# Optimization experiments

Measured on AMD Instinct MI355X. Metric: run time of the kernel, lower is better.

The kernel has to match this reference:

```python
import jax, jax.numpy as jnp
import numpy as np

DILATION = 1
THETA = 1.0
K = 3 + 2 * (DILATION - 1)  # 3x3 window


def setup_inputs() -> dict:
    key = jax.random.key(0)
    x = jax.random.normal(key, (8, 64, 224, 224), dtype=jnp.float32)
    return {"x": x}


def _extract_patches(x, k, d):
    # x: [b, c, h, w] -> patches: [b, c, k*k, h, w], zero-padded like F.unfold(padding=d)
    b, c, h, w = x.shape
    xp = jnp.pad(x, ((0, 0), (0, 0), (d, d), (d, d)))
    return jnp.stack(
        [xp[:, :, i * d:i * d + h, j * d:j * d + w] for i in range(k) for j in range(k)],
        axis=2,
    )


def reference(x) -> jnp.ndarray:
    b, c, h, w = x.shape
    patches = _extract_patches(x, K, DILATION)  # [b, c, kk, h, w]

    mean = patches.mean(axis=2, keepdims=True)
    # torch .std() is unbiased (ddof=1)
    std = jnp.clip(jnp.std(patches, axis=2, keepdims=True, ddof=1), 1e-3, None)
    normed = (patches - mean) / std

    contrast = (normed ** 2).mean(axis=2)
    energy = (patches ** 2).mean(axis=2)
    clamped = jnp.clip(patches, 1e-6, None)
    entropy = -(clamped * jnp.log(clamped)).mean(axis=2)
    homogeneity = 1.0 / ((1.0 + jnp.abs(patches - mean)).mean(axis=2) + 1e-6)

    feats = jnp.stack([contrast, energy, entropy, homogeneity], axis=2)  # [b, c, 4, h, w]

    log_feat = jnp.log(jnp.clip(feats, 1e-5, None))
    martingale = jnp.clip(jnp.exp(THETA * log_feat - 0.5 * THETA ** 2), 1e-4, 1e4)
    martingale = jnp.where(jnp.isfinite(martingale), martingale, jnp.ones_like(martingale))

    # per-channel feature stacks concatenated along channel dim -> [b, c*4, h, w]
    return martingale.reshape(b, c * 4, h, w)
```

## Files before the change

kernel.cpp:

```cpp
#include <hip/hip_runtime.h>
#include <math.h>

#define B 8
#define C 64
#define H 224
#define W 224
#define TW 32
#define TH 8

__global__ __launch_bounds__(256) void medseg_kernel(const float* __restrict__ x,
                                                     float* __restrict__ out) {
    __shared__ float tile[(TH + 2)][(TW + 2)];

    const int plane = blockIdx.z;
    const int w0 = blockIdx.x * TW;
    const int h0 = blockIdx.y * TH;
    const float* __restrict__ xp = x + (size_t)plane * (H * W);

    const int tid = threadIdx.x;

    #pragma unroll
    for (int i = tid; i < (TH + 2) * (TW + 2); i += 256) {
        const int r  = i / (TW + 2);
        const int cc = i - r * (TW + 2);
        const int hh = h0 + r - 1;
        const int ww = w0 + cc - 1;
        float v = 0.0f;
        if (hh >= 0 && hh < H && ww >= 0 && ww < W) v = xp[hh * W + ww];
        tile[r][cc] = v;
    }
    __syncthreads();

    const int tx = tid & (TW - 1);
    const int ty = tid >> 5;

    float v[9];
    #pragma unroll
    for (int i = 0; i < 3; ++i)
        #pragma unroll
        for (int j = 0; j < 3; ++j)
            v[i * 3 + j] = tile[ty + i][tx + j];

    float s1 = 0.0f, s2 = 0.0f;
    #pragma unroll
    for (int k = 0; k < 9; ++k) {
        s1 += v[k];
        s2 = fmaf(v[k], v[k], s2);
    }
    const float mean = s1 * (1.0f / 9.0f);

    float s2c = 0.0f, sad = 0.0f;
    #pragma unroll
    for (int k = 0; k < 9; ++k) {
        const float d = v[k] - mean;
        s2c = fmaf(d, d, s2c);
        sad += fabsf(d);
    }

    float st = 0.0f;
    #pragma unroll
    for (int k = 0; k < 9; ++k) {
        const float c = fmaxf(v[k], 1e-6f);
        st = fmaf(c, __logf(c), st);
    }

    const float var  = s2c * (1.0f / 8.0f);
    const float stdc = fmaxf(__fsqrt_rn(var), 1e-3f);

    const float contrast = (s2c / (stdc * stdc)) * (1.0f / 9.0f);
    const float energy   = s2 * (1.0f / 9.0f);
    const float entropy  = -st * (1.0f / 9.0f);
    const float homog    = 1.0f / (1.0f + sad * (1.0f / 9.0f) + 1e-6f);

    const float EXPM = 0.6065306597126334f;
    float m[4];
    m[0] = contrast; m[1] = energy; m[2] = entropy; m[3] = homog;
    #pragma unroll
    for (int f = 0; f < 4; ++f) {
        float mm = fmaxf(m[f], 1e-5f) * EXPM;
        mm = fminf(fmaxf(mm, 1e-4f), 1e4f);
        if (!isfinite(mm)) mm = 1.0f;
        m[f] = mm;
    }

    const size_t base = ((size_t)plane * 4) * (size_t)(H * W)
                      + (size_t)(h0 + ty) * W + (w0 + tx);
    #pragma unroll
    for (int f = 0; f < 4; ++f) {
        out[base + (size_t)f * (H * W)] = m[f];
    }
}

extern "C" void kernel_launch(void* const* d_in, const int* in_sizes, int n_in,
                              void* d_out, int out_size, void* d_ws, size_t ws_size,
                              hipStream_t stream) {
    const float* x = (const float*)d_in[0];
    float* out = (float*)d_out;
    dim3 grid(W / TW, H / TH, B * C);
    dim3 block(TW * TH);
    medseg_kernel<<<grid, block, 0, stream>>>(x, out);
}
```

Before: 554.2 us.

## Compute four outputs per thread with register sliding window and float4 I/O

Drops the shared-memory tile and barrier. Each thread now loads three float4 chunks per row for three rows straight into registers and computes four horizontally adjacent outputs. Column sums of values, squares and x·log(x) are shared between neighbouring windows, so the per-element log is computed once per column rather than once per window. Outputs are written as float4. The cost is more redundant global loads for halos and higher register pressure, with launch_bounds set to 4 blocks.

```diff
diff --git a/kernel.cpp b/kernel.cpp
--- a/kernel.cpp
+++ b/kernel.cpp
@@ -5,90 +5,93 @@
 #define C 64
 #define H 224
 #define W 224
+#define HW (H * W)
 #define TW 32
-#define TH 8
+#define TH 32
 
-__global__ __launch_bounds__(256) void medseg_kernel(const float* __restrict__ x,
-                                                     float* __restrict__ out) {
-    __shared__ float tile[(TH + 2)][(TW + 2)];
-
+__global__ __launch_bounds__(256, 4) void medseg_kernel(const float* __restrict__ x,
+                                                        float* __restrict__ out) {
     const int plane = blockIdx.z;
     const int w0 = blockIdx.x * TW;
     const int h0 = blockIdx.y * TH;
-    const float* __restrict__ xp = x + (size_t)plane * (H * W);
+    const int tid = threadIdx.x;
+    const int tx = tid & 7;
+    const int ty = tid >> 3;
 
-    const int tid = threadIdx.x;
+    const float* __restrict__ xp = x + (size_t)plane * HW;
+
+    const int cb = w0 + 4 * tx;
+    const int h  = h0 + ty;
+
+    float win[3][12];
+    const float4 Z = make_float4(0.f, 0.f, 0.f, 0.f);
+    #pragma unroll
+    for (int i = 0; i < 3; ++i) {
+        const int r = h - 1 + i;
+        const bool rin = (r >= 0) && (r < H);
+        const float* rowp = xp + r * W;
+        float4 a = (rin && cb > 0)     ? *(const float4*)(rowp + cb - 4) : Z;
+        float4 b = rin                 ? *(const float4*)(rowp + cb)     : Z;
+        float4 c = (rin && cb + 4 < W) ? *(const float4*)(rowp + cb + 4) : Z;
+        win[i][0] = a.x; win[i][1]  = a.y; win[i][2]  = a.z; win[i][3]  = a.w;
+        win[i][4] = b.x; win[i][5]  = b.y; win[i][6]  = b.z; win[i][7]  = b.w;
+        win[i][8] = c.x; win[i][9]  = c.y; win[i][10] = c.z; win[i][11] = c.w;
+    }
+
+    float cs[6], cq[6], ce[6];
+    #pragma unroll
+    for (int j = 0; j < 6; ++j) {
+        const float v0 = win[0][j + 3], v1 = win[1][j + 3], v2 = win[2][j + 3];
+        cs[j] = v0 + v1 + v2;
+        cq[j] = fmaf(v0, v0, fmaf(v1, v1, v2 * v2));
+        const float c0 = fmaxf(v0, 1e-6f), c1 = fmaxf(v1, 1e-6f), c2 = fmaxf(v2, 1e-6f);
+        ce[j] = fmaf(c0, __logf(c0), fmaf(c1, __logf(c1), c2 * __logf(c2)));
+    }
+
+    const float EXPM = 0.6065306597126334f;
+    float oc[4], oe[4], ot[4], oh[4];
 
     #pragma unroll
-    for (int i = tid; i < (TH + 2) * (TW + 2); i += 256) {
-        const int r  = i / (TW + 2);
-        const int cc = i - r * (TW + 2);
-        const int hh = h0 + r - 1;
-        const int ww = w0 + cc - 1;
-        float v = 0.0f;
-        if (hh >= 0 && hh < H && ww >= 0 && ww < W) v = xp[hh * W + ww];
-        tile[r][cc] = v;
-    }
-    __syncthreads();
+    for (int k = 0; k < 4; ++k) {
+        const float s1  = cs[k] + cs[k + 1] + cs[k + 2];
+        const float s2  = cq[k] + cq[k + 1] + cq[k + 2];
+        const float se  = ce[k] + ce[k + 1] + ce[k + 2];
+        const float mean = s1 * (1.0f / 9.0f);
 
-    const int tx = tid & (TW - 1);
-    const int ty = tid >> 5;
+        float s2c = 0.0f, sad = 0.0f;
+        #pragma unroll
+        for (int i = 0; i < 3; ++i)
+            #pragma unroll
+            for (int j = 0; j < 3; ++j) {
+                const float d = win[i][k + j + 3] - mean;
+                s2c = fmaf(d, d, s2c);
+                sad += fabsf(d);
+            }
 
-    float v[9];
-    #pragma unroll
-    for (int i = 0; i < 3; ++i)
-        #pragma unroll
-        for (int j = 0; j < 3; ++j)
-            v[i * 3 + j] = tile[ty + i][tx + j];
+        const float var  = s2c * (1.0f / 8.0f);
+        const float stdc = fmaxf(__fsqrt_rn(var), 1e-3f);
 
-    float s1 = 0.0f, s2 = 0.0f;
-    #pragma unroll
-    for (int k = 0; k < 9; ++k) {
-        s1 += v[k];
-        s2 = fmaf(v[k], v[k], s2);
-    }
-    const float mean = s1 * (1.0f / 9.0f);
+        float m0 = (s2c / (stdc * stdc)) * (1.0f / 9.0f);
+        float m1 = s2 * (1.0f / 9.0f);
+        float m2 = -se * (1.0f / 9.0f);
+        float m3 = 1.0f / (1.0f + sad * (1.0f / 9.0f) + 1e-6f);
 
-    float s2c = 0.0f, sad = 0.0f;
-    #pragma unroll
-    for (int k = 0; k < 9; ++k) {
-        const float d = v[k] - mean;
-        s2c = fmaf(d, d, s2c);
-        sad += fabsf(d);
+        #define MART(mm) do {                                   \
+            mm = fmaxf(mm, 1e-5f) * EXPM;                       \
+            mm = fminf(fmaxf(mm, 1e-4f), 1e4f);                 \
+            if (!isfinite(mm)) mm = 1.0f;                       \
+        } while (0)
+        MART(m0); MART(m1); MART(m2); MART(m3);
+        #undef MART
+
+        oc[k] = m0; oe[k] = m1; ot[k] = m2; oh[k] = m3;
     }
 
-    float st = 0.0f;
-    #pragma unroll
-    for (int k = 0; k < 9; ++k) {
-        const float c = fmaxf(v[k], 1e-6f);
-        st = fmaf(c, __logf(c), st);
-    }
-
-    const float var  = s2c * (1.0f / 8.0f);
-    const float stdc = fmaxf(__fsqrt_rn(var), 1e-3f);
-
-    const float contrast = (s2c / (stdc * stdc)) * (1.0f / 9.0f);
-    const float energy   = s2 * (1.0f / 9.0f);
-    const float entropy  = -st * (1.0f / 9.0f);
-    const float homog    = 1.0f / (1.0f + sad * (1.0f / 9.0f) + 1e-6f);
-
-    const float EXPM = 0.6065306597126334f;
-    float m[4];
-    m[0] = contrast; m[1] = energy; m[2] = entropy; m[3] = homog;
-    #pragma unroll
-    for (int f = 0; f < 4; ++f) {
-        float mm = fmaxf(m[f], 1e-5f) * EXPM;
-        mm = fminf(fmaxf(mm, 1e-4f), 1e4f);
-        if (!isfinite(mm)) mm = 1.0f;
-        m[f] = mm;
-    }
-
-    const size_t base = ((size_t)plane * 4) * (size_t)(H * W)
-                      + (size_t)(h0 + ty) * W + (w0 + tx);
-    #pragma unroll
-    for (int f = 0; f < 4; ++f) {
-        out[base + (size_t)f * (H * W)] = m[f];
-    }
+    float* ob = out + ((size_t)plane * 4) * HW + (size_t)h * W + cb;
+    *(float4*)(ob + 0 * HW) = make_float4(oc[0], oc[1], oc[2], oc[3]);
+    *(float4*)(ob + 1 * HW) = make_float4(oe[0], oe[1], oe[2], oe[3]);
+    *(float4*)(ob + 2 * HW) = make_float4(ot[0], ot[1], ot[2], ot[3]);
+    *(float4*)(ob + 3 * HW) = make_float4(oh[0], oh[1], oh[2], oh[3]);
 }
 
 extern "C" void kernel_launch(void* const* d_in, const int* in_sizes, int n_in,
@@ -97,6 +100,6 @@
     const float* x = (const float*)d_in[0];
     float* out = (float*)d_out;
     dim3 grid(W / TW, H / TH, B * C);
-    dim3 block(TW * TH);
+    dim3 block(256);
     medseg_kernel<<<grid, block, 0, stream>>>(x, out);
 }
```

Result: no change. 545.3 us (-1.6%).
